# Kernel optimization log

Hardware: AMD Instinct MI355X
Metric: run time of the kernel (lower is better)

Reference implementation:

```python
import jax, jax.numpy as jnp
import numpy as np
from jax import lax

T_STEPS = 4
TAU = 2.0
V_THRESHOLD = 1.0
V_RESET = 0.0
ATAN_ALPHA = 2.0

@jax.custom_vjp
def atan_spike(x):
    # Heaviside forward, ATan surrogate gradient (spikingjelly surrogate.ATan, alpha=2)
    return (x >= 0.0).astype(x.dtype)

def _atan_fwd(x):
    return atan_spike(x), x

def _atan_bwd(x, g):
    grad = (ATAN_ALPHA / 2.0) / (1.0 + (jnp.pi / 2.0 * ATAN_ALPHA * x) ** 2)
    return (g * grad,)

atan_spike.defvjp(_atan_fwd, _atan_bwd)

def setup_inputs() -> dict:
    key = jax.random.key(0)
    inputs = jax.random.normal(key, (32, 720, 862), dtype=jnp.float32)  # B, L, C
    return {"inputs": inputs}

def reference(inputs) -> jnp.ndarray:
    # repeat along a new leading time dim: (T, B, L, C)
    x = jnp.broadcast_to(inputs[None], (T_STEPS,) + inputs.shape)
    # permute(0,1,3,2) -> (T, B, C, L)
    x = jnp.transpose(x, (0, 1, 3, 2))

    def step(v, xt):
        # LIF with decay_input=True (spikingjelly default):
        # v <- v + (x - (v - v_reset)) / tau
        v = v + (xt - (v - V_RESET)) / TAU
        s = atan_spike(v - V_THRESHOLD)
        sd = lax.stop_gradient(s)  # detach_reset=True
        v = (1.0 - sd) * v + sd * V_RESET  # hard reset
        return v, s

    v0 = jnp.zeros_like(x[0])
    _, spks = lax.scan(step, v0, x)
    return spks  # (T, B, C, L)
```

## Files before the change

kernel.cpp:

```cpp
#include <hip/hip_runtime.h>


#define B_DIM 32
#define L_DIM 720
#define C_DIM 862
#define T_STEPS 4
#define TC 16
#define SL 724

typedef float v2f __attribute__((ext_vector_type(2)));
typedef float v4f __attribute__((ext_vector_type(4)));

__global__ __launch_bounds__(256)
void lif_repeat_encoder(const float* __restrict__ in, float* __restrict__ out) {
    __shared__ float sm[TC * SL];

    const int b   = blockIdx.y;
    const int c0  = blockIdx.x * TC;
    const int tid = threadIdx.x;

    const float* __restrict__ inb = in + (size_t)b * (L_DIM * C_DIM);

    {
        const int cl2 = (tid & 7) << 1;
        const int c   = c0 + cl2;
        const int r0  = tid >> 3;
        if (c < C_DIM) {
            for (int base = 0; base < L_DIM; base += 128) {
                v2f v[4];
#pragma unroll
                for (int u = 0; u < 4; ++u) {
                    const int r = base + r0 + 32 * u;
                    if (r < L_DIM)
                        v[u] = *(const v2f*)(inb + (size_t)r * C_DIM + c);
                }
#pragma unroll
                for (int u = 0; u < 4; ++u) {
                    const int r = base + r0 + 32 * u;
                    if (r < L_DIM) {
                        sm[cl2 * SL + r]       = v[u].x;
                        sm[(cl2 + 1) * SL + r] = v[u].y;
                    }
                }
            }
        }
    }
    __syncthreads();

    const int wave = tid >> 6;
    const int lane = tid & 63;
    const size_t plane = (size_t)B_DIM * C_DIM * L_DIM;

#pragma unroll
    for (int q = 0; q < 4; ++q) {
        const int cl = wave * 4 + q;
        const int c  = c0 + cl;
        if (c >= C_DIM) continue;

        const size_t rowbase = ((size_t)b * C_DIM + c) * L_DIM;

#pragma unroll
        for (int round = 0; round < 3; ++round) {
            const int j = lane + 64 * round;
            if (j >= L_DIM / 4) break;

            const v4f x = *(const v4f*)(sm + cl * SL + 4 * j);

            float sx[T_STEPS], sy[T_STEPS], sz[T_STEPS], sw[T_STEPS];
            float v0 = 0.f, v1 = 0.f, v2 = 0.f, v3 = 0.f;
#pragma unroll
            for (int t = 0; t < T_STEPS; ++t) {
                v0 += (x.x - v0) * 0.5f;
                v1 += (x.y - v1) * 0.5f;
                v2 += (x.z - v2) * 0.5f;
                v3 += (x.w - v3) * 0.5f;
                sx[t] = (v0 >= 1.0f) ? 1.0f : 0.0f;
                sy[t] = (v1 >= 1.0f) ? 1.0f : 0.0f;
                sz[t] = (v2 >= 1.0f) ? 1.0f : 0.0f;
                sw[t] = (v3 >= 1.0f) ? 1.0f : 0.0f;
                v0 = (v0 >= 1.0f) ? 0.0f : v0;
                v1 = (v1 >= 1.0f) ? 0.0f : v1;
                v2 = (v2 >= 1.0f) ? 0.0f : v2;
                v3 = (v3 >= 1.0f) ? 0.0f : v3;
            }

#pragma unroll
            for (int t = 0; t < T_STEPS; ++t) {
                v4f o;
                o.x = sx[t]; o.y = sy[t]; o.z = sz[t]; o.w = sw[t];
                *(v4f*)(out + (size_t)t * plane + rowbase + 4 * j) = o;
            }
        }
    }
}

extern "C" void kernel_launch(void* const* d_in, const int* in_sizes, int n_in,
                              void* d_out, int out_size, void* d_ws, size_t ws_size,
                              hipStream_t stream) {
    const float* in = (const float*)d_in[0];
    float* out = (float*)d_out;

    dim3 block(256, 1, 1);
    dim3 grid((C_DIM + TC - 1) / TC,
              B_DIM,
              1);

    lif_repeat_encoder<<<grid, block, 0, stream>>>(in, out);
}
```

Measured before the change: 377.6 us.

## Compute LIF spikes during load and stage packed spike bytes in LDS

The LIF recurrence now runs at load time, and each element's four spike bits are packed into one byte that goes to shared memory instead of the float input. This cuts LDS footprint and bandwidth by four and may allow more resident blocks. The store phase reads all packed words into registers first, then writes by time step, so each output plane is written as a contiguous sweep. Risks are byte-granular LDS stores with possible bank conflicts and slightly higher register use. The kernel stays bound by global output writes.

Result: no change. 374.9 us (-0.7%).

```diff
diff --git a/kernel.cpp b/kernel.cpp
--- a/kernel.cpp
+++ b/kernel.cpp
@@ -6,14 +6,25 @@
 #define C_DIM 862
 #define T_STEPS 4
 #define TC 16
-#define SL 724
+#define SLB 724
 
 typedef float v2f __attribute__((ext_vector_type(2)));
 typedef float v4f __attribute__((ext_vector_type(4)));
 
+__device__ __forceinline__ unsigned lif_spike_byte(float x) {
+    float v = 0.0f;
+    unsigned b = 0;
+#pragma unroll
+    for (int t = 0; t < T_STEPS; ++t) {
+        v += (x - v) * 0.5f;
+        if (v >= 1.0f) { b |= (1u << t); v = 0.0f; }
+    }
+    return b;
+}
+
 __global__ __launch_bounds__(256)
 void lif_repeat_encoder(const float* __restrict__ in, float* __restrict__ out) {
-    __shared__ float sm[TC * SL];
+    __shared__ unsigned char sl[TC * SLB];
 
     const int b   = blockIdx.y;
     const int c0  = blockIdx.x * TC;
@@ -38,8 +49,8 @@
                 for (int u = 0; u < 4; ++u) {
                     const int r = base + r0 + 32 * u;
                     if (r < L_DIM) {
-                        sm[cl2 * SL + r]       = v[u].x;
-                        sm[(cl2 + 1) * SL + r] = v[u].y;
+                        sl[cl2 * SLB + r]       = (unsigned char)lif_spike_byte(v[u].x);
+                        sl[(cl2 + 1) * SLB + r] = (unsigned char)lif_spike_byte(v[u].y);
                     }
                 }
             }
@@ -49,46 +60,39 @@
 
     const int wave = tid >> 6;
     const int lane = tid & 63;
+
+    unsigned sp[4][3];
+#pragma unroll
+    for (int q = 0; q < 4; ++q) {
+#pragma unroll
+        for (int round = 0; round < 3; ++round) {
+            const int j = lane + 64 * round;
+            const int cl = 4 * wave + q;
+            sp[q][round] = (j < L_DIM / 4)
+                ? *(const unsigned*)(sl + cl * SLB + 4 * j) : 0u;
+        }
+    }
+
     const size_t plane = (size_t)B_DIM * C_DIM * L_DIM;
 
 #pragma unroll
-    for (int q = 0; q < 4; ++q) {
-        const int cl = wave * 4 + q;
-        const int c  = c0 + cl;
-        if (c >= C_DIM) continue;
-
-        const size_t rowbase = ((size_t)b * C_DIM + c) * L_DIM;
-
+    for (int t = 0; t < T_STEPS; ++t) {
 #pragma unroll
-        for (int round = 0; round < 3; ++round) {
-            const int j = lane + 64 * round;
-            if (j >= L_DIM / 4) break;
-
-            const v4f x = *(const v4f*)(sm + cl * SL + 4 * j);
-
-            float sx[T_STEPS], sy[T_STEPS], sz[T_STEPS], sw[T_STEPS];
-            float v0 = 0.f, v1 = 0.f, v2 = 0.f, v3 = 0.f;
+        for (int q = 0; q < 4; ++q) {
+            const int c = c0 + 4 * wave + q;
+            if (c >= C_DIM) continue;
+            float* dst = out + (size_t)t * plane + ((size_t)b * C_DIM + c) * L_DIM;
 #pragma unroll
-            for (int t = 0; t < T_STEPS; ++t) {
-                v0 += (x.x - v0) * 0.5f;
-                v1 += (x.y - v1) * 0.5f;
-                v2 += (x.z - v2) * 0.5f;
-                v3 += (x.w - v3) * 0.5f;
-                sx[t] = (v0 >= 1.0f) ? 1.0f : 0.0f;
-                sy[t] = (v1 >= 1.0f) ? 1.0f : 0.0f;
-                sz[t] = (v2 >= 1.0f) ? 1.0f : 0.0f;
-                sw[t] = (v3 >= 1.0f) ? 1.0f : 0.0f;
-                v0 = (v0 >= 1.0f) ? 0.0f : v0;
-                v1 = (v1 >= 1.0f) ? 0.0f : v1;
-                v2 = (v2 >= 1.0f) ? 0.0f : v2;
-                v3 = (v3 >= 1.0f) ? 0.0f : v3;
-            }
-
-#pragma unroll
-            for (int t = 0; t < T_STEPS; ++t) {
+            for (int round = 0; round < 3; ++round) {
+                const int j = lane + 64 * round;
+                if (j >= L_DIM / 4) break;
+                const unsigned y = (sp[q][round] >> t) & 0x01010101u;
                 v4f o;
-                o.x = sx[t]; o.y = sy[t]; o.z = sz[t]; o.w = sw[t];
-                *(v4f*)(out + (size_t)t * plane + rowbase + 4 * j) = o;
+                o.x = (float)(y & 1u);
+                o.y = (float)((y >> 8) & 1u);
+                o.z = (float)((y >> 16) & 1u);
+                o.w = (float)((y >> 24) & 1u);
+                *(v4f*)(dst + 4 * j) = o;
             }
         }
     }
```
